# Kernel tuning notes

Measured on AMD Instinct MI355X. Metric: run time of the kernel, lower is better.

## Reference

```python
import jax, jax.numpy as jnp
import numpy as np


def _consts(n_fft):
    # Static index/twiddle tables, mirroring FastIMDCT4.__init__ (numpy, host-side).
    N4 = n_fft // 4
    k = np.arange(N4)
    pre0 = 2 * k                       # even taps
    pre1 = n_fft // 2 - 1 - 2 * k      # reversed odd taps
    tw = np.exp(-2j * np.pi / n_fft * (k.astype(np.float32) + 0.125)).astype(np.complex64)
    # post-FFT de-interleave index (length n_fft, values in [0, n_fft//2))
    idx = np.empty(n_fft, np.int64)
    idx[0:n_fft // 2:2] = np.arange(0, n_fft // 2, 2)
    idx[1:n_fft // 2:2] = np.arange(n_fft // 2 - 1, 0, -2)
    idx[n_fft // 2:] = idx[:n_fft // 2][::-1]
    post = np.roll(idx, -n_fft // 4)
    # sign pattern folded into the window
    sign = np.ones(n_fft, np.float64)
    sign[1::2] *= -1.0
    sign[:n_fft // 4] *= -1.0
    sign = np.roll(sign, -n_fft // 4)
    return pre0, pre1, tw, post, sign


def setup_inputs() -> dict:
    key = jax.random.key(0)
    B, T, n_fft, hop = 32, 1024, 2048, 1024
    signal = jax.random.normal(key, (B, T, n_fft // 2), dtype=jnp.float32)
    window = jnp.ones((n_fft,), dtype=jnp.float32)  # raw window (module default: ones)
    return {"signal": signal, "window": window, "n_fft": n_fft, "hop_length": hop}


def reference(signal, window, n_fft, hop_length):
    pre0, pre1, tw, post, sign = _consts(n_fft)
    # combined window: 4 * sign * window / n_fft (module precomputes this in __init__)
    win = (4.0 * jnp.asarray(sign, jnp.float32) * window / n_fft)
    # pre-twiddle gather -> complex [B, T, n_fft//4]
    c = signal[..., pre0] + 1j * signal[..., pre1]
    twj = jnp.asarray(tw)
    c = twj * c
    c = jnp.fft.fft(c, axis=-1)
    c = twj * c
    B, T = c.shape[0], c.shape[1]
    # interleave real/imag -> [B, T, n_fft//2], then post gather -> [B, T, n_fft]
    inter = jnp.stack([jnp.real(c), jnp.imag(c)], axis=-1).reshape(B, T, n_fft // 2)
    frames = win * inter[..., post]            # [B, T, n_fft]
    # overlap-add fold (F.fold with kernel (1, n_fft), stride (1, hop))
    out_len = (T - 1) * hop_length + n_fft
    pos = (np.arange(T)[:, None] * hop_length + np.arange(n_fft)[None, :]).reshape(-1)
    out = jnp.zeros((B, out_len), frames.dtype).at[:, pos].add(frames.reshape(B, -1))
    # center=True trimming
    out = out[:, n_fft // 2: -(n_fft // 2)]
    return out[:, None, None, :]               # [B, 1, 1, (T-1)*hop], matches fold output layout
```

## Files before the change

### kernel.cpp

```cpp
#include <hip/hip_runtime.h>


#define CHUNKS 1023
#define CPB 7
#define BPB 147

__device__ __forceinline__ float2 cmul(float2 a, float2 b) {
    return make_float2(a.x * b.x - a.y * b.y, a.x * b.y + a.y * b.x);
}
__device__ __forceinline__ float2 cadd(float2 a, float2 b) {
    return make_float2(a.x + b.x, a.y + b.y);
}
__device__ __forceinline__ float2 csub(float2 a, float2 b) {
    return make_float2(a.x - b.x, a.y - b.y);
}
__device__ __forceinline__ float2 twid(float rev) {
    return make_float2(__builtin_amdgcn_cosf(rev), __builtin_amdgcn_sinf(rev));
}

__device__ __forceinline__ void postmap(int m, int& p, float& sgn) {
    bool even = ((m & 1) == 0);
    if (m < 512)       p = even ? (m + 512)  : (512 - m);
    else if (m < 1536) p = even ? (m - 511)  : (1535 - m);
    else               p = even ? (m - 1536) : (2560 - m);
    float s1 = even ? 1.0f : -1.0f;
    sgn = (m < 1536) ? s1 : -s1;
}

__device__ __forceinline__ int brev3(int r) {
    return ((r & 1) << 2) | (r & 2) | ((r >> 2) & 1);
}

__device__ __forceinline__ void radix8(float2 c[8]) {
    const float RH = 0.70710678118654752f;
    {
        float2 u0 = c[0], u1 = c[1], u2 = c[2], u3 = c[3];
        float2 l0 = c[4], l1 = c[5], l2 = c[6], l3 = c[7];
        float2 t1 = csub(u1, l1), t2 = csub(u2, l2), t3 = csub(u3, l3);
        c[0] = cadd(u0, l0); c[4] = csub(u0, l0);
        c[1] = cadd(u1, l1); c[5] = cmul(make_float2(RH, -RH), t1);
        c[2] = cadd(u2, l2); c[6] = make_float2(t2.y, -t2.x);
        c[3] = cadd(u3, l3); c[7] = cmul(make_float2(-RH, -RH), t3);
    }
    #pragma unroll
    for (int b = 0; b < 8; b += 4) {
        float2 u0 = c[b], u1 = c[b + 1], d0 = c[b + 2], d1 = c[b + 3];
        float2 t = csub(u1, d1);
        c[b] = cadd(u0, d0);
        c[b + 2] = csub(u0, d0);
        c[b + 1] = cadd(u1, d1);
        c[b + 3] = make_float2(t.y, -t.x);
    }
    #pragma unroll
    for (int b = 0; b < 8; b += 2) {
        float2 u = c[b], d = c[b + 1];
        c[b] = cadd(u, d); c[b + 1] = csub(u, d);
    }
}

__device__ __forceinline__ void midchain(float2 c[8], float2 w) {
    float2 wc = w;
    c[4] = cmul(wc, c[4]);
    wc = cmul(wc, w); c[2] = cmul(wc, c[2]);
    wc = cmul(wc, w); c[6] = cmul(wc, c[6]);
    wc = cmul(wc, w); c[1] = cmul(wc, c[1]);
    wc = cmul(wc, w); c[5] = cmul(wc, c[5]);
    wc = cmul(wc, w); c[3] = cmul(wc, c[3]);
    wc = cmul(wc, w); c[7] = cmul(wc, c[7]);
}

#define K32_DECL \
    const float K32C[8] = {1.0f, 0.98078528040323044913f, 0.92387953251128675613f, \
                           0.83146961230254523708f, 0.70710678118654752440f,       \
                           0.55557023301960222474f, 0.38268343236508977173f,       \
                           0.19509032201612826785f};                               \
    const float K32S[8] = {0.0f, -0.19509032201612826785f, -0.38268343236508977173f,\
                           -0.55557023301960222474f, -0.70710678118654752440f,     \
                           -0.83146961230254523708f, -0.92387953251128675613f,     \
                           -0.98078528040323044913f};

__device__ __forceinline__ void fft_frame(const float* __restrict__ row, int lane,
                                          float* __restrict__ planes,
                                          const float2* __restrict__ T1b,
                                          const float2* __restrict__ TM,
                                          const float2* __restrict__ TM2,
                                          const float2* __restrict__ TP2) {
    K32_DECL
    const float2* row2 = (const float2*)row;
    float2* scratch = (float2*)planes;
    const int lh = lane >> 3;
    const int ll = lane & 7;

    float2 v[8];
    #pragma unroll
    for (int r = 0; r < 8; ++r) v[r] = row2[64 * r + lane];

    float2 base = T1b[lane];
    float2 c[8];
    #pragma unroll
    for (int r = 0; r < 8; ++r) {
        float im = __shfl_xor(v[7 - r].y, 63);
        float2 tw = (r == 0) ? base : cmul(base, make_float2(K32C[r], K32S[r]));
        c[r] = cmul(tw, make_float2(v[r].x, im));
    }

    radix8(c);
    midchain(c, TM[lane]);

    #pragma unroll
    for (int r = 0; r < 8; ++r) {
        const int q = brev3(r);
        scratch[q * 64 + ((lh ^ q)) * 8 + ll] = c[r];
    }
    asm volatile("" ::: "memory");
    #pragma unroll
    for (int r = 0; r < 8; ++r)
        c[r] = scratch[lh * 64 + ((r ^ lh)) * 8 + ll];

    radix8(c);
    midchain(c, TM2[ll]);

    #pragma unroll
    for (int r = 0; r < 8; ++r) {
        const int j1 = brev3(r);
        scratch[lh * 64 + ((j1 ^ lh)) * 8 + (ll ^ j1)] = c[r];
    }
    asm volatile("" ::: "memory");
    #pragma unroll
    for (int r = 0; r < 8; ++r)
        c[r] = scratch[lh * 64 + ((ll ^ lh)) * 8 + (r ^ ll)];

    radix8(c);

    float2 base2 = TP2[lane];
    const int kbase = 8 * ll + lh;
    #pragma unroll
    for (int j = 0; j < 8; ++j) {
        float2 tw = (j == 0) ? base2 : cmul(base2, make_float2(K32C[j], K32S[j]));
        float2 dv = cmul(tw, c[brev3(j)]);
        planes[64 * j + kbase]       = dv.x;
        planes[512 + 64 * j + kbase] = dv.y;
    }
}

__global__ __launch_bounds__(512) void imdct_kernel(
        const float* __restrict__ signal,
        const float* __restrict__ window,
        float* __restrict__ out) {
    __shared__ float lds[8][1024];
    __shared__ float2 T1b[64];
    __shared__ float2 TM[64];
    __shared__ float2 TP2[64];
    __shared__ float2 TM2[8];

    const int tid = threadIdx.x;
    const int lane = tid & 63;
    const int w = tid >> 6;

    if (tid < 64) {
        T1b[tid] = twid(-((float)tid + 0.125f) * (1.0f / 2048.0f));
        TM[tid]  = twid(-(float)tid * (1.0f / 512.0f));
        TP2[tid] = twid(-((float)(8 * (tid & 7) + (tid >> 3)) + 0.125f) * (1.0f / 2048.0f));
    }
    if (tid < 8) TM2[tid] = twid(-(float)tid * (1.0f / 64.0f));
    __syncthreads();

    const int bid = blockIdx.x;
    const int b = bid / BPB;
    const int cblk = bid - b * BPB;
    const int q0 = cblk * CPB;

    const int f = q0 + w;
    if (f <= 1023) {
        fft_frame(signal + (size_t)(b * 1024 + f) * 1024, lane, &lds[w][0],
                  T1b, TM, TM2, TP2);
    }
    __syncthreads();

    float* orow_base = out + (size_t)b * (CHUNKS * 1024);
    const int r = 2 * tid;

    int p00, p01, p10, p11; float s00, s01, s10, s11;
    postmap(1024 + r,     p00, s00);
    postmap(1024 + r + 1, p01, s01);
    postmap(r,            p10, s10);
    postmap(r + 1,        p11, s11);
    const float2 wh = *(const float2*)(window + 1024 + r);
    const float2 wl = *(const float2*)(window + r);
    const float a00 = s00 * wh.x * (1.0f / 512.0f);
    const float a01 = s01 * wh.y * (1.0f / 512.0f);
    const float a10 = s10 * wl.x * (1.0f / 512.0f);
    const float a11 = s11 * wl.y * (1.0f / 512.0f);
    const int o00 = (p00 & 1) * 512 + (p00 >> 1);
    const int o01 = (p01 & 1) * 512 + (p01 >> 1);
    const int o10 = (p10 & 1) * 512 + (p10 >> 1);
    const int o11 = (p11 & 1) * 512 + (p11 >> 1);

    #pragma unroll
    for (int j = 0; j < CPB; ++j) {
        const int qj = q0 + j;
        if (qj > 1022) break;
        const float* f0 = &lds[j][0];
        const float* f1 = &lds[j + 1][0];
        float2 o;
        o.x = a00 * f0[o00] + a10 * f1[o10];
        o.y = a01 * f0[o01] + a11 * f1[o11];
        *(float2*)(orow_base + (size_t)qj * 1024 + r) = o;
    }
}

extern "C" void kernel_launch(void* const* d_in, const int* in_sizes, int n_in,
                              void* d_out, int out_size, void* d_ws, size_t ws_size,
                              hipStream_t stream) {
    const float* signal = (const float*)d_in[0];
    const float* window = (const float*)d_in[1];
    float* out = (float*)d_out;
    imdct_kernel<<<dim3(32 * BPB), dim3(512), 0, stream>>>(signal, window, out);
}
```

Baseline: 236.4 us.

## Make IMDCT kernel persistent with register prefetch of the next frame group

Replaces the one-block-per-frame-group launch with a fixed grid of 1024 persistent blocks that loop over groups. Each block issues global loads for its next group's frame into registers before the overlap-add stores of the current group, so load latency overlaps with LDS work and stores. Explicit barriers with an LDS waitcnt order the FFT writes against the overlap-add reads. The cost is fewer resident blocks and extra barriers per iteration. One twiddle constant literal is also altered, but the change falls below float precision.

```diff
diff --git a/kernel.cpp b/kernel.cpp
--- a/kernel.cpp
+++ b/kernel.cpp
@@ -4,6 +4,8 @@
 #define CHUNKS 1023
 #define CPB 7
 #define BPB 147
+#define NGROUPS (32 * BPB)
+#define GRID 1024
 
 __device__ __forceinline__ float2 cmul(float2 a, float2 b) {
     return make_float2(a.x * b.x - a.y * b.y, a.x * b.y + a.y * b.x);
@@ -76,24 +78,26 @@
                            0.19509032201612826785f};                               \
     const float K32S[8] = {0.0f, -0.19509032201612826785f, -0.38268343236508977173f,\
                            -0.55557023301960222474f, -0.70710678118654752440f,     \
-                           -0.83146961230254523708f, -0.92387953251128675613f,     \
+                           -0.83146961230254752440f, -0.92387953251128675613f,     \
                            -0.98078528040323044913f};
 
-__device__ __forceinline__ void fft_frame(const float* __restrict__ row, int lane,
-                                          float* __restrict__ planes,
-                                          const float2* __restrict__ T1b,
-                                          const float2* __restrict__ TM,
-                                          const float2* __restrict__ TM2,
-                                          const float2* __restrict__ TP2) {
+__device__ __forceinline__ void load_frame(const float* __restrict__ row, int lane,
+                                           float2 v[8]) {
+    const float2* row2 = (const float2*)row;
+    #pragma unroll
+    for (int r = 0; r < 8; ++r) v[r] = row2[64 * r + lane];
+}
+
+__device__ __forceinline__ void fft_from_regs(const float2 v[8], int lane,
+                                              float* __restrict__ planes,
+                                              const float2* __restrict__ T1b,
+                                              const float2* __restrict__ TM,
+                                              const float2* __restrict__ TM2,
+                                              const float2* __restrict__ TP2) {
     K32_DECL
-    const float2* row2 = (const float2*)row;
     float2* scratch = (float2*)planes;
     const int lh = lane >> 3;
     const int ll = lane & 7;
-
-    float2 v[8];
-    #pragma unroll
-    for (int r = 0; r < 8; ++r) v[r] = row2[64 * r + lane];
 
     float2 base = T1b[lane];
     float2 c[8];
@@ -110,12 +114,12 @@
     #pragma unroll
     for (int r = 0; r < 8; ++r) {
         const int q = brev3(r);
-        scratch[q * 64 + ((lh ^ q)) * 8 + ll] = c[r];
+        scratch[q * 64 + (lh ^ q) * 8 + ll] = c[r];
     }
     asm volatile("" ::: "memory");
     #pragma unroll
     for (int r = 0; r < 8; ++r)
-        c[r] = scratch[lh * 64 + ((r ^ lh)) * 8 + ll];
+        c[r] = scratch[lh * 64 + (r ^ lh) * 8 + ll];
 
     radix8(c);
     midchain(c, TM2[ll]);
@@ -123,12 +127,12 @@
     #pragma unroll
     for (int r = 0; r < 8; ++r) {
         const int j1 = brev3(r);
-        scratch[lh * 64 + ((j1 ^ lh)) * 8 + (ll ^ j1)] = c[r];
+        scratch[lh * 64 + (j1 ^ lh) * 8 + (ll ^ j1)] = c[r];
     }
     asm volatile("" ::: "memory");
     #pragma unroll
     for (int r = 0; r < 8; ++r)
-        c[r] = scratch[lh * 64 + ((ll ^ lh)) * 8 + (r ^ ll)];
+        c[r] = scratch[lh * 64 + (ll ^ lh) * 8 + (r ^ ll)];
 
     radix8(c);
 
@@ -163,23 +167,8 @@
         TP2[tid] = twid(-((float)(8 * (tid & 7) + (tid >> 3)) + 0.125f) * (1.0f / 2048.0f));
     }
     if (tid < 8) TM2[tid] = twid(-(float)tid * (1.0f / 64.0f));
-    __syncthreads();
-
-    const int bid = blockIdx.x;
-    const int b = bid / BPB;
-    const int cblk = bid - b * BPB;
-    const int q0 = cblk * CPB;
-
-    const int f = q0 + w;
-    if (f <= 1023) {
-        fft_frame(signal + (size_t)(b * 1024 + f) * 1024, lane, &lds[w][0],
-                  T1b, TM, TM2, TP2);
-    }
-    __syncthreads();
-
-    float* orow_base = out + (size_t)b * (CHUNKS * 1024);
+
     const int r = 2 * tid;
-
     int p00, p01, p10, p11; float s00, s01, s10, s11;
     postmap(1024 + r,     p00, s00);
     postmap(1024 + r + 1, p01, s01);
@@ -196,16 +185,53 @@
     const int o10 = (p10 & 1) * 512 + (p10 >> 1);
     const int o11 = (p11 & 1) * 512 + (p11 >> 1);
 
-    #pragma unroll
-    for (int j = 0; j < CPB; ++j) {
-        const int qj = q0 + j;
-        if (qj > 1022) break;
-        const float* f0 = &lds[j][0];
-        const float* f1 = &lds[j + 1][0];
-        float2 o;
-        o.x = a00 * f0[o00] + a10 * f1[o10];
-        o.y = a01 * f0[o01] + a11 * f1[o11];
-        *(float2*)(orow_base + (size_t)qj * 1024 + r) = o;
+    int g = blockIdx.x;
+    int b = g / BPB;
+    int q0 = (g - b * BPB) * CPB;
+    bool act = (q0 + w <= 1023);
+    float2 v[8];
+    if (act) load_frame(signal + (size_t)(b * 1024 + q0 + w) * 1024, lane, v);
+    __syncthreads();
+
+    for (;;) {
+        if (act) fft_from_regs(v, lane, &lds[w][0], T1b, TM, TM2, TP2);
+
+        const int gn = g + GRID;
+        const bool have_next = (gn < NGROUPS);
+        int bn = b, qn0 = q0; bool actn = false;
+        if (have_next) {
+            bn = gn / BPB;
+            qn0 = (gn - bn * BPB) * CPB;
+            actn = (qn0 + w <= 1023);
+            if (actn) load_frame(signal + (size_t)(bn * 1024 + qn0 + w) * 1024, lane, v);
+        }
+
+        __builtin_amdgcn_sched_barrier(0);
+        asm volatile("s_waitcnt lgkmcnt(0)" ::: "memory");
+        __builtin_amdgcn_sched_barrier(0);
+        __builtin_amdgcn_s_barrier();
+        asm volatile("" ::: "memory");
+
+        float* orow_base = out + (size_t)b * (CHUNKS * 1024);
+        #pragma unroll
+        for (int j = 0; j < CPB; ++j) {
+            const int qj = q0 + j;
+            if (qj > 1022) break;
+            const float* f0 = &lds[j][0];
+            const float* f1 = &lds[j + 1][0];
+            float2 o;
+            o.x = a00 * f0[o00] + a10 * f1[o10];
+            o.y = a01 * f0[o01] + a11 * f1[o11];
+            *(float2*)(orow_base + (size_t)qj * 1024 + r) = o;
+        }
+
+        if (!have_next) break;
+
+        asm volatile("" ::: "memory");
+        __builtin_amdgcn_s_barrier();
+        asm volatile("" ::: "memory");
+
+        g = gn; b = bn; q0 = qn0; act = actn;
     }
 }
 
@@ -215,5 +241,5 @@
     const float* signal = (const float*)d_in[0];
     const float* window = (const float*)d_in[1];
     float* out = (float*)d_out;
-    imdct_kernel<<<dim3(32 * BPB), dim3(512), 0, stream>>>(signal, window, out);
-}
+    imdct_kernel<<<dim3(GRID), dim3(512), 0, stream>>>(signal, window, out);
+}
```

Result: slower. 248.9 us (+5.3%).

## Shrink blocks to 4 frames and prefetch frame loads before twiddle setup

Applied to the files above, without the earlier changes.

Blocks now handle 3 output chunks with 4 wavefronts (256 threads) instead of 7 chunks with 8 wavefronts, which removes the idle 8th frame and the tail bounds checks since 1023 = 3*341. The signal load is issued before the twiddle-table setup and the first barrier so global latency overlaps table computation and postmap index precomputation. Each thread now writes two float2 outputs per chunk. The trade-off is more redundant overlap frames per block: each block computes 4 FFTs for 3 chunks instead of 8 for 7, so FFT work rises by roughly a sixth.

```diff
diff --git a/kernel.cpp b/kernel.cpp
--- a/kernel.cpp
+++ b/kernel.cpp
@@ -2,8 +2,9 @@
 
 
 #define CHUNKS 1023
-#define CPB 7
-#define BPB 147
+#define CPB 3
+#define GPB 341
+#define GRID (32 * GPB)
 
 __device__ __forceinline__ float2 cmul(float2 a, float2 b) {
     return make_float2(a.x * b.x - a.y * b.y, a.x * b.y + a.y * b.x);
@@ -79,30 +80,34 @@
                            -0.83146961230254523708f, -0.92387953251128675613f,     \
                            -0.98078528040323044913f};
 
-__device__ __forceinline__ void fft_frame(const float* __restrict__ row, int lane,
-                                          float* __restrict__ planes,
-                                          const float2* __restrict__ T1b,
-                                          const float2* __restrict__ TM,
-                                          const float2* __restrict__ TM2,
-                                          const float2* __restrict__ TP2) {
+__device__ __forceinline__ void load_frame(const float* __restrict__ row, int lane,
+                                           float2 v[8]) {
+    const float2* row2 = (const float2*)row;
+    #pragma unroll
+    for (int r = 0; r < 8; ++r) v[r] = row2[64 * r + lane];
+}
+
+__device__ __forceinline__ void fft_pre(const float2 v[8], int lane, float2 c[8],
+                                        const float2* __restrict__ T1b) {
     K32_DECL
-    const float2* row2 = (const float2*)row;
-    float2* scratch = (float2*)planes;
-    const int lh = lane >> 3;
-    const int ll = lane & 7;
-
-    float2 v[8];
-    #pragma unroll
-    for (int r = 0; r < 8; ++r) v[r] = row2[64 * r + lane];
-
     float2 base = T1b[lane];
-    float2 c[8];
     #pragma unroll
     for (int r = 0; r < 8; ++r) {
         float im = __shfl_xor(v[7 - r].y, 63);
         float2 tw = (r == 0) ? base : cmul(base, make_float2(K32C[r], K32S[r]));
         c[r] = cmul(tw, make_float2(v[r].x, im));
     }
+}
+
+__device__ __forceinline__ void fft_rest(float2 c[8], int lane,
+                                         float* __restrict__ planes,
+                                         const float2* __restrict__ TM,
+                                         const float2* __restrict__ TM2,
+                                         const float2* __restrict__ TP2) {
+    K32_DECL
+    float2* scratch = (float2*)planes;
+    const int lh = lane >> 3;
+    const int ll = lane & 7;
 
     radix8(c);
     midchain(c, TM[lane]);
@@ -110,12 +115,12 @@
     #pragma unroll
     for (int r = 0; r < 8; ++r) {
         const int q = brev3(r);
-        scratch[q * 64 + ((lh ^ q)) * 8 + ll] = c[r];
+        scratch[q * 64 + (lh ^ q) * 8 + ll] = c[r];
     }
     asm volatile("" ::: "memory");
     #pragma unroll
     for (int r = 0; r < 8; ++r)
-        c[r] = scratch[lh * 64 + ((r ^ lh)) * 8 + ll];
+        c[r] = scratch[lh * 64 + (r ^ lh) * 8 + ll];
 
     radix8(c);
     midchain(c, TM2[ll]);
@@ -123,12 +128,12 @@
     #pragma unroll
     for (int r = 0; r < 8; ++r) {
         const int j1 = brev3(r);
-        scratch[lh * 64 + ((j1 ^ lh)) * 8 + (ll ^ j1)] = c[r];
+        scratch[lh * 64 + (j1 ^ lh) * 8 + (ll ^ j1)] = c[r];
     }
     asm volatile("" ::: "memory");
     #pragma unroll
     for (int r = 0; r < 8; ++r)
-        c[r] = scratch[lh * 64 + ((ll ^ lh)) * 8 + (r ^ ll)];
+        c[r] = scratch[lh * 64 + (ll ^ lh) * 8 + (r ^ ll)];
 
     radix8(c);
 
@@ -143,11 +148,11 @@
     }
 }
 
-__global__ __launch_bounds__(512) void imdct_kernel(
+__global__ __launch_bounds__(256) void imdct_kernel(
         const float* __restrict__ signal,
         const float* __restrict__ window,
         float* __restrict__ out) {
-    __shared__ float lds[8][1024];
+    __shared__ float lds[4][1024];
     __shared__ float2 T1b[64];
     __shared__ float2 TM[64];
     __shared__ float2 TP2[64];
@@ -157,55 +162,82 @@
     const int lane = tid & 63;
     const int w = tid >> 6;
 
+    const int bid = blockIdx.x;
+    const int b = bid / GPB;
+    const int gb = bid - b * GPB;
+    const int q0 = gb * CPB;
+
+    float2 v[8];
+    load_frame(signal + (size_t)(b * 1024 + q0 + w) * 1024, lane, v);
+
     if (tid < 64) {
         T1b[tid] = twid(-((float)tid + 0.125f) * (1.0f / 2048.0f));
         TM[tid]  = twid(-(float)tid * (1.0f / 512.0f));
         TP2[tid] = twid(-((float)(8 * (tid & 7) + (tid >> 3)) + 0.125f) * (1.0f / 2048.0f));
     }
     if (tid < 8) TM2[tid] = twid(-(float)tid * (1.0f / 64.0f));
+
+    float aA00, aA01, aA10, aA11, aB00, aB01, aB10, aB11;
+    unsigned poA0, poA1, poB0, poB1;
+    {
+        const int rA = 2 * tid;
+        const int rB = rA + 512;
+        int p; float s;
+        unsigned o;
+        postmap(1024 + rA, p, s);     o  = (p & 1) * 512 + (p >> 1);
+        aA00 = s;                     poA0 = o;
+        postmap(1024 + rA + 1, p, s); o  = (p & 1) * 512 + (p >> 1);
+        aA01 = s;                     poA0 |= o << 16;
+        postmap(rA, p, s);            o  = (p & 1) * 512 + (p >> 1);
+        aA10 = s;                     poA1 = o;
+        postmap(rA + 1, p, s);        o  = (p & 1) * 512 + (p >> 1);
+        aA11 = s;                     poA1 |= o << 16;
+        postmap(1024 + rB, p, s);     o  = (p & 1) * 512 + (p >> 1);
+        aB00 = s;                     poB0 = o;
+        postmap(1024 + rB + 1, p, s); o  = (p & 1) * 512 + (p >> 1);
+        aB01 = s;                     poB0 |= o << 16;
+        postmap(rB, p, s);            o  = (p & 1) * 512 + (p >> 1);
+        aB10 = s;                     poB1 = o;
+        postmap(rB + 1, p, s);        o  = (p & 1) * 512 + (p >> 1);
+        aB11 = s;                     poB1 |= o << 16;
+
+        const float2 whA = *(const float2*)(window + 1024 + rA);
+        const float2 wlA = *(const float2*)(window + rA);
+        const float2 whB = *(const float2*)(window + 1024 + rB);
+        const float2 wlB = *(const float2*)(window + rB);
+        aA00 *= whA.x * (1.0f / 512.0f);  aA01 *= whA.y * (1.0f / 512.0f);
+        aA10 *= wlA.x * (1.0f / 512.0f);  aA11 *= wlA.y * (1.0f / 512.0f);
+        aB00 *= whB.x * (1.0f / 512.0f);  aB01 *= whB.y * (1.0f / 512.0f);
+        aB10 *= wlB.x * (1.0f / 512.0f);  aB11 *= wlB.y * (1.0f / 512.0f);
+    }
     __syncthreads();
 
-    const int bid = blockIdx.x;
-    const int b = bid / BPB;
-    const int cblk = bid - b * BPB;
-    const int q0 = cblk * CPB;
-
-    const int f = q0 + w;
-    if (f <= 1023) {
-        fft_frame(signal + (size_t)(b * 1024 + f) * 1024, lane, &lds[w][0],
-                  T1b, TM, TM2, TP2);
+    {
+        float2 c[8];
+        fft_pre(v, lane, c, T1b);
+        fft_rest(c, lane, &lds[w][0], TM, TM2, TP2);
     }
     __syncthreads();
 
-    float* orow_base = out + (size_t)b * (CHUNKS * 1024);
-    const int r = 2 * tid;
-
-    int p00, p01, p10, p11; float s00, s01, s10, s11;
-    postmap(1024 + r,     p00, s00);
-    postmap(1024 + r + 1, p01, s01);
-    postmap(r,            p10, s10);
-    postmap(r + 1,        p11, s11);
-    const float2 wh = *(const float2*)(window + 1024 + r);
-    const float2 wl = *(const float2*)(window + r);
-    const float a00 = s00 * wh.x * (1.0f / 512.0f);
-    const float a01 = s01 * wh.y * (1.0f / 512.0f);
-    const float a10 = s10 * wl.x * (1.0f / 512.0f);
-    const float a11 = s11 * wl.y * (1.0f / 512.0f);
-    const int o00 = (p00 & 1) * 512 + (p00 >> 1);
-    const int o01 = (p01 & 1) * 512 + (p01 >> 1);
-    const int o10 = (p10 & 1) * 512 + (p10 >> 1);
-    const int o11 = (p11 & 1) * 512 + (p11 >> 1);
+    const int oA00 = poA0 & 0xFFFF, oA01 = poA0 >> 16;
+    const int oA10 = poA1 & 0xFFFF, oA11 = poA1 >> 16;
+    const int oB00 = poB0 & 0xFFFF, oB01 = poB0 >> 16;
+    const int oB10 = poB1 & 0xFFFF, oB11 = poB1 >> 16;
+    const int rA = 2 * tid;
+    float* orow_base = out + (size_t)b * (CHUNKS * 1024) + (size_t)q0 * 1024;
 
     #pragma unroll
     for (int j = 0; j < CPB; ++j) {
-        const int qj = q0 + j;
-        if (qj > 1022) break;
         const float* f0 = &lds[j][0];
         const float* f1 = &lds[j + 1][0];
-        float2 o;
-        o.x = a00 * f0[o00] + a10 * f1[o10];
-        o.y = a01 * f0[o01] + a11 * f1[o11];
-        *(float2*)(orow_base + (size_t)qj * 1024 + r) = o;
+        float2 o0, o1;
+        o0.x = aA00 * f0[oA00] + aA10 * f1[oA10];
+        o0.y = aA01 * f0[oA01] + aA11 * f1[oA11];
+        o1.x = aB00 * f0[oB00] + aB10 * f1[oB10];
+        o1.y = aB01 * f0[oB01] + aB11 * f1[oB11];
+        float* orow = orow_base + (size_t)j * 1024;
+        *(float2*)(orow + rA)       = o0;
+        *(float2*)(orow + rA + 512) = o1;
     }
 }
 
@@ -215,5 +247,5 @@
     const float* signal = (const float*)d_in[0];
     const float* window = (const float*)d_in[1];
     float* out = (float*)d_out;
-    imdct_kernel<<<dim3(32 * BPB), dim3(512), 0, stream>>>(signal, window, out);
-}
+    imdct_kernel<<<dim3(GRID), dim3(256), 0, stream>>>(signal, window, out);
+}
```

New measurement: 232.8 us. Within noise of the previous version (-1.5%).
